# Kernel optimization log

Hardware: AMD Instinct MI355X
Metric: run time of the kernel (lower is better)

## Reference

```python
import jax, jax.numpy as jnp
import numpy as np

B, T, D = 4096, 8, 2048
EPS = 1e-5


def setup_inputs() -> dict:
    key = jax.random.key(0)
    ks = jax.random.split(key, 7)
    s = 1.0 / np.sqrt(D)  # xavier-ish scale
    return {
        "H": jax.random.normal(ks[0], (B, T, D), jnp.float32),
        "Wq": jax.random.normal(ks[1], (T, D, D), jnp.float32) * s,
        "Wk": jax.random.normal(ks[2], (D, D), jnp.float32) * s,
        "Wv": jax.random.normal(ks[3], (D, D), jnp.float32) * s,
        "Wg": jax.random.normal(ks[4], (T, D, D), jnp.float32) * s,
        "bg": jnp.zeros((T, D), jnp.float32),
        "gamma": jnp.ones((T, D), jnp.float32),
        "beta": jnp.zeros((T, D), jnp.float32),
    }


def reference(H, Wq, Wk, Wv, Wg, bg, gamma, beta):
    # H: (B, T, D) = stacked task_reprs. Linear uses y = x @ W.T.
    scale = jnp.sqrt(jnp.asarray(D, H.dtype))
    K = jnp.einsum('bsd,ed->bse', H, Wk)          # (B, T, D) shared keys
    V = jnp.einsum('bsd,ed->bse', H, Wv)          # (B, T, D) shared values
    Q = jnp.einsum('btd,ted->bte', H, Wq)         # per-task query projection
    scores = jnp.einsum('bte,bse->bts', Q, K) / scale  # (B, T, T)
    attn = jax.nn.softmax(scores, axis=-1)
    ctx = jnp.einsum('bts,bse->bte', attn, V)     # (B, T, D)
    # dropout is identity at eval time
    g = jax.nn.sigmoid(jnp.einsum('btd,ted->bte', H, Wg) + bg)  # per-task gate
    x = H + g * ctx                               # gated residual
    mu = jnp.mean(x, axis=-1, keepdims=True)
    var = jnp.var(x, axis=-1, keepdims=True)
    out = (x - mu) / jnp.sqrt(var + EPS) * gamma + beta  # per-task LayerNorm
    return out
```

## Files before the change

### kernel.cpp

```cpp
#include <hip/hip_runtime.h>
#include <cstdint>

typedef unsigned short u16;
typedef uint32_t u32;
typedef float f32x4 __attribute__((ext_vector_type(4)));
typedef __bf16 bf16x8 __attribute__((ext_vector_type(8)));

#define GLDS16(gp, lp)                                                                   \
  __builtin_amdgcn_global_load_lds((const __attribute__((address_space(1))) void*)(gp),  \
                                   (__attribute__((address_space(3))) void*)(lp), 16, 0, 0)

__device__ __forceinline__ float blo(u32 u) { return __uint_as_float(u << 16); }
__device__ __forceinline__ float bhi(u32 u) { return __uint_as_float(u & 0xFFFF0000u); }
__device__ __forceinline__ u16 f2b(float f) {
  u32 u = __float_as_uint(f);
  u32 r = u + 0x7FFFu + ((u >> 16) & 1u);
  return (u16)(r >> 16);
}

__global__ __launch_bounds__(256) void ctil_cvt_f2b(
    const float* __restrict__ in, u16* __restrict__ out, long n)
{
  long i = ((long)blockIdx.x * blockDim.x + threadIdx.x) * 8;
  const long stride = (long)gridDim.x * blockDim.x * 8;
  for (; i < n; i += stride) {
    float4 a = *reinterpret_cast<const float4*>(in + i);
    float4 b = *reinterpret_cast<const float4*>(in + i + 4);
    uint4 o;
    o.x = (u32)f2b(a.x) | ((u32)f2b(a.y) << 16);
    o.y = (u32)f2b(a.z) | ((u32)f2b(a.w) << 16);
    o.z = (u32)f2b(b.x) | ((u32)f2b(b.y) << 16);
    o.w = (u32)f2b(b.z) | ((u32)f2b(b.w) << 16);
    *reinterpret_cast<uint4*>(out + i) = o;
  }
}

__global__ __launch_bounds__(512, 2) void ctil_gemm256(
    const u16* __restrict__ Hb, const u16* __restrict__ Wqb,
    const u16* __restrict__ Wkb, const u16* __restrict__ Wvb,
    const u16* __restrict__ Wgb,
    u16* __restrict__ Kb, u16* __restrict__ Vb,
    u16* __restrict__ Qb, u16* __restrict__ Gb,
    int zbase)
{
  const int z = blockIdx.z + zbase;
  const u16* A;
  const u16* W;
  u16* C;
  int lda, ldc;
  if (z < 2) {
    A = Hb; lda = 2048; ldc = 2048;
    W = (z == 0) ? Wkb : Wvb;
    C = (z == 0) ? Kb : Vb;
  } else {
    const int t = (z - 2) & 7;
    A = Hb + t * 2048; lda = 16384; ldc = 16384;
    W = ((z < 10) ? Wqb : Wgb) + (size_t)t * (size_t)(2048 * 2048);
    C = ((z < 10) ? Qb : Gb) + t * 2048;
  }
  const int bm = blockIdx.x, bn = blockIdx.y;

  const int tid = (int)threadIdx.x;
  const int lane = tid & 63, wid = tid >> 6;
  const int wm = wid >> 2, wn = wid & 3;

  __shared__ __align__(16) u16 As[2][16384];
  __shared__ __align__(16) u16 Bs[2][16384];

  const int srl = lane >> 3;
  const int sq  = (lane & 7) ^ srl;
  const u16* Ag = A + (size_t)(bm * 256 + wid * 8 + srl) * lda + sq * 8;
  const u16* Bg = W + (size_t)(bn * 256 + wid * 8 + srl) * 2048 + sq * 8;

#define STAGE(buf, kt, h)                                                     \
  do {                                                                        \
    GLDS16(Ag + (size_t)((h) * 64) * lda + (kt) * 64,                         \
           &As[buf][((h) * 64 + wid * 8) * 64]);                              \
    GLDS16(Bg + (size_t)((h) * 64) * 2048 + (kt) * 64,                        \
           &Bs[buf][((h) * 64 + wid * 8) * 64]);                              \
  } while (0)

  const int la = lane & 15, g = lane >> 4, x = lane & 7;
  const int arow = wm * 128 + la;
  const int brow = wn * 64 + la;
  const int sl0 = (g ^ x) << 3;
  const int sl1 = ((4 | g) ^ x) << 3;

  bf16x8 aR[4][2];
  bf16x8 bR[2][2][2];
  f32x4 acc[8][4] = {};

#define DSA(buf, mh)                                                          \
  do {                                                                        \
    _Pragma("unroll") for (int j = 0; j < 4; ++j) {                           \
      const int r_ = (arow + (mh) * 64 + j * 16) * 64;                        \
      aR[j][0] = *reinterpret_cast<const bf16x8*>(&As[buf][r_ + sl0]);        \
      aR[j][1] = *reinterpret_cast<const bf16x8*>(&As[buf][r_ + sl1]);        \
    }                                                                         \
  } while (0)

#define DSB(buf, nh)                                                          \
  do {                                                                        \
    _Pragma("unroll") for (int j = 0; j < 2; ++j) {                           \
      const int r_ = (brow + (nh) * 32 + j * 16) * 64;                        \
      bR[nh][j][0] = *reinterpret_cast<const bf16x8*>(&Bs[buf][r_ + sl0]);    \
      bR[nh][j][1] = *reinterpret_cast<const bf16x8*>(&Bs[buf][r_ + sl1]);    \
    }                                                                         \
  } while (0)

#define MFMA16(mh, nh)                                                        \
  do {                                                                        \
    _Pragma("unroll") for (int j = 0; j < 4; ++j)                             \
    _Pragma("unroll") for (int jj = 0; jj < 2; ++jj)                          \
    _Pragma("unroll") for (int ks = 0; ks < 2; ++ks)                          \
      acc[(mh) * 4 + j][(nh) * 2 + jj] =                                      \
          __builtin_amdgcn_mfma_f32_16x16x32_bf16(                            \
              aR[j][ks], bR[nh][jj][ks], acc[(mh) * 4 + j][(nh) * 2 + jj],    \
              0, 0, 0);                                                       \
  } while (0)

#define BAR()                                                                 \
  do {                                                                        \
    __builtin_amdgcn_s_barrier();                                             \
    asm volatile("" ::: "memory");                                            \
  } while (0)
#define LGKMW() asm volatile("s_waitcnt lgkmcnt(0)" ::: "memory")
#define VMW(n) asm volatile("s_waitcnt vmcnt(" #n ")" ::: "memory")
#define PRIO_ON()  __builtin_amdgcn_s_setprio(1)
#define PRIO_OFF() __builtin_amdgcn_s_setprio(0)

#pragma unroll
  for (int h = 0; h < 4; ++h) STAGE(0, 0, h);
  STAGE(1, 1, 0);
  STAGE(1, 1, 1);
  VMW(4);
  BAR();

#pragma unroll 1
  for (int it = 0; it < 16; ++it) {
    const int k1 = 2 * it + 1, k2 = 2 * it + 2, k3 = 2 * it + 3;
    const bool nl = (it < 15);
    DSA(0, 0); DSB(0, 0);
    STAGE(1, k1, 2);
    STAGE(1, k1, 3);
    PRIO_ON(); MFMA16(0, 0); PRIO_OFF();
    BAR();
    DSB(0, 1);
    PRIO_ON(); MFMA16(0, 1); PRIO_OFF();
    BAR();
    DSA(0, 1);
    PRIO_ON(); MFMA16(1, 1); PRIO_OFF();
    LGKMW();
    BAR();
    if (nl) { STAGE(0, k2, 0); STAGE(0, k2, 1); }
    PRIO_ON(); MFMA16(1, 0); PRIO_OFF();
    if (nl) VMW(4); else VMW(0);
    BAR();
    DSA(1, 0); DSB(1, 0);
    if (nl) { STAGE(0, k2, 2); STAGE(0, k2, 3); }
    PRIO_ON(); MFMA16(0, 0); PRIO_OFF();
    BAR();
    DSB(1, 1);
    PRIO_ON(); MFMA16(0, 1); PRIO_OFF();
    BAR();
    DSA(1, 1);
    PRIO_ON(); MFMA16(1, 1); PRIO_OFF();
    LGKMW();
    BAR();
    if (nl) { STAGE(1, k3, 0); STAGE(1, k3, 1); }
    PRIO_ON(); MFMA16(1, 0); PRIO_OFF();
    if (nl) VMW(4); else VMW(0);
    BAR();
  }

  const int cl = lane & 15, cq = lane >> 4;
#pragma unroll
  for (int mf = 0; mf < 8; ++mf) {
#pragma unroll
    for (int r = 0; r < 4; ++r) {
      const int row = bm * 256 + wm * 128 + mf * 16 + cq * 4 + r;
      u16* Cr = C + (size_t)row * ldc + bn * 256 + wn * 64 + cl;
#pragma unroll
      for (int nf = 0; nf < 4; ++nf)
        Cr[nf * 16] = f2b(acc[mf][nf][r]);
    }
  }
#undef STAGE
#undef DSA
#undef DSB
#undef MFMA16
#undef BAR
#undef LGKMW
#undef VMW
}

__global__ __launch_bounds__(256) void ctil_epilogue(
    const u16* __restrict__ Hb, const u16* __restrict__ Kb,
    const u16* __restrict__ Vb, const u16* __restrict__ Qb,
    const u16* __restrict__ Gb, const float* __restrict__ bgp,
    const float* __restrict__ gap, const float* __restrict__ bep,
    float* __restrict__ Out)
{
  const int b = blockIdx.x;
  const int tid = (int)threadIdx.x;
  const int lane = tid & 63, wid = tid >> 6;
  const size_t rbase = (size_t)b * 16384;
  const int e0 = tid * 8;

  __shared__ float red[256];
  __shared__ float r1s[4], r2s[4];

  u32 qw[8][4], kw[8][4];
#pragma unroll
  for (int t = 0; t < 8; ++t) {
    uint4 v = *reinterpret_cast<const uint4*>(Qb + rbase + t * 2048 + e0);
    qw[t][0] = v.x; qw[t][1] = v.y; qw[t][2] = v.z; qw[t][3] = v.w;
    uint4 w = *reinterpret_cast<const uint4*>(Kb + rbase + t * 2048 + e0);
    kw[t][0] = w.x; kw[t][1] = w.y; kw[t][2] = w.z; kw[t][3] = w.w;
  }

  float sc[64];
#pragma unroll
  for (int p = 0; p < 64; ++p) sc[p] = 0.f;

#pragma unroll
  for (int c = 0; c < 4; ++c) {
    float ql[8], qh[8], kl[8], kh[8];
#pragma unroll
    for (int t = 0; t < 8; ++t) {
      ql[t] = blo(qw[t][c]); qh[t] = bhi(qw[t][c]);
      kl[t] = blo(kw[t][c]); kh[t] = bhi(kw[t][c]);
    }
#pragma unroll
    for (int t = 0; t < 8; ++t)
#pragma unroll
      for (int s = 0; s < 8; ++s)
        sc[t * 8 + s] += ql[t] * kl[s] + qh[t] * kh[s];
  }

#pragma unroll
  for (int p = 0; p < 64; ++p) {
    float v = sc[p];
#pragma unroll
    for (int m = 1; m < 64; m <<= 1) v += __shfl_xor(v, m, 64);
    sc[p] = v;
  }
  if (lane == 0) {
#pragma unroll
    for (int p = 0; p < 64; ++p) red[wid * 64 + p] = sc[p];
  }
  __syncthreads();

  const float INVS = 0.022097086912079608f;
#pragma unroll
  for (int p = 0; p < 64; ++p)
    sc[p] = (red[p] + red[64 + p] + red[128 + p] + red[192 + p]) * INVS;

#pragma unroll
  for (int t = 0; t < 8; ++t) {
    float m = sc[t * 8];
#pragma unroll
    for (int s = 1; s < 8; ++s) m = fmaxf(m, sc[t * 8 + s]);
    float l = 0.f;
#pragma unroll
    for (int s = 0; s < 8; ++s) {
      float e = __expf(sc[t * 8 + s] - m);
      sc[t * 8 + s] = e;
      l += e;
    }
    float inv = 1.f / l;
#pragma unroll
    for (int s = 0; s < 8; ++s) sc[t * 8 + s] *= inv;
  }

  u32 vw[8][4];
#pragma unroll
  for (int s = 0; s < 8; ++s) {
    uint4 v = *reinterpret_cast<const uint4*>(Vb + rbase + s * 2048 + e0);
    vw[s][0] = v.x; vw[s][1] = v.y; vw[s][2] = v.z; vw[s][3] = v.w;
  }

  for (int t = 0; t < 8; ++t) {
    float cx[8];
#pragma unroll
    for (int j = 0; j < 8; ++j) cx[j] = 0.f;
#pragma unroll
    for (int s = 0; s < 8; ++s) {
      float a = sc[t * 8 + s];
#pragma unroll
      for (int c = 0; c < 4; ++c) {
        cx[2 * c]     += a * blo(vw[s][c]);
        cx[2 * c + 1] += a * bhi(vw[s][c]);
      }
    }
    uint4 gu = *reinterpret_cast<const uint4*>(Gb + rbase + t * 2048 + e0);
    uint4 hu = *reinterpret_cast<const uint4*>(Hb + rbase + t * 2048 + e0);
    u32 ga[4] = {gu.x, gu.y, gu.z, gu.w};
    u32 ha[4] = {hu.x, hu.y, hu.z, hu.w};
    float bgv[8];
    *reinterpret_cast<float4*>(&bgv[0]) = *reinterpret_cast<const float4*>(bgp + t * 2048 + e0);
    *reinterpret_cast<float4*>(&bgv[4]) = *reinterpret_cast<const float4*>(bgp + t * 2048 + e0 + 4);
    float x[8];
    float s1 = 0.f, s2 = 0.f;
#pragma unroll
    for (int c = 0; c < 4; ++c) {
      float gl = blo(ga[c]) + bgv[2 * c];
      float gh = bhi(ga[c]) + bgv[2 * c + 1];
      float sgl = 1.f / (1.f + __expf(-gl));
      float sgh = 1.f / (1.f + __expf(-gh));
      float xl = blo(ha[c]) + sgl * cx[2 * c];
      float xh = bhi(ha[c]) + sgh * cx[2 * c + 1];
      x[2 * c] = xl; x[2 * c + 1] = xh;
      s1 += xl + xh;
      s2 += xl * xl + xh * xh;
    }
#pragma unroll
    for (int m = 1; m < 64; m <<= 1) {
      s1 += __shfl_xor(s1, m, 64);
      s2 += __shfl_xor(s2, m, 64);
    }
    if (lane == 0) { r1s[wid] = s1; r2s[wid] = s2; }
    __syncthreads();
    const float invD = 1.f / 2048.f;
    float S1 = r1s[0] + r1s[1] + r1s[2] + r1s[3];
    float S2 = r2s[0] + r2s[1] + r2s[2] + r2s[3];
    float mu = S1 * invD;
    float var = S2 * invD - mu * mu;
    float rstd = rsqrtf(var + 1e-5f);
    float gmv[8], btv[8];
    *reinterpret_cast<float4*>(&gmv[0]) = *reinterpret_cast<const float4*>(gap + t * 2048 + e0);
    *reinterpret_cast<float4*>(&gmv[4]) = *reinterpret_cast<const float4*>(gap + t * 2048 + e0 + 4);
    *reinterpret_cast<float4*>(&btv[0]) = *reinterpret_cast<const float4*>(bep + t * 2048 + e0);
    *reinterpret_cast<float4*>(&btv[4]) = *reinterpret_cast<const float4*>(bep + t * 2048 + e0 + 4);
    float4 o1, o2;
    o1.x = (x[0] - mu) * rstd * gmv[0] + btv[0];
    o1.y = (x[1] - mu) * rstd * gmv[1] + btv[1];
    o1.z = (x[2] - mu) * rstd * gmv[2] + btv[2];
    o1.w = (x[3] - mu) * rstd * gmv[3] + btv[3];
    o2.x = (x[4] - mu) * rstd * gmv[4] + btv[4];
    o2.y = (x[5] - mu) * rstd * gmv[5] + btv[5];
    o2.z = (x[6] - mu) * rstd * gmv[6] + btv[6];
    o2.w = (x[7] - mu) * rstd * gmv[7] + btv[7];
    *reinterpret_cast<float4*>(Out + rbase + t * 2048 + e0) = o1;
    *reinterpret_cast<float4*>(Out + rbase + t * 2048 + e0 + 4) = o2;
    __syncthreads();
  }
}

extern "C" void kernel_launch(void* const* d_in, const int* in_sizes, int n_in,
                              void* d_out, int out_size, void* d_ws, size_t ws_size,
                              hipStream_t stream)
{
  const float* H  = (const float*)d_in[0];
  const float* Wq = (const float*)d_in[1];
  const float* Wk = (const float*)d_in[2];
  const float* Wv = (const float*)d_in[3];
  const float* Wg = (const float*)d_in[4];
  const float* bg = (const float*)d_in[5];
  const float* ga = (const float*)d_in[6];
  const float* be = (const float*)d_in[7];
  float* Out = (float*)d_out;

  const size_t NWQ = 33554432, NWK = 4194304;
  u16* Wqb = (u16*)d_ws;
  u16* Wgb = Wqb + NWQ;
  u16* Wkb = Wgb + NWQ;
  u16* Wvb = Wkb + NWK;
  u16* chunkbase = Wvb + NWK;

  const size_t fixed = 150994944ull;
  int nch = 1;
  while (nch < 16 && fixed + (size_t)(4096 / nch) * 163840ull > ws_size) nch <<= 1;
  const int CB = 4096 / nch;

  u16* Hb = chunkbase;
  u16* Kw = Hb + (size_t)CB * 16384;
  u16* Vw = Kw + (size_t)CB * 16384;
  u16* Gw = Vw + (size_t)CB * 16384;
  u16* Qw = Gw + (size_t)CB * 16384;

  ctil_cvt_f2b<<<2048, 256, 0, stream>>>(Wq, Wqb, (long)NWQ);
  ctil_cvt_f2b<<<2048, 256, 0, stream>>>(Wg, Wgb, (long)NWQ);
  ctil_cvt_f2b<<<512, 256, 0, stream>>>(Wk, Wkb, (long)NWK);
  ctil_cvt_f2b<<<512, 256, 0, stream>>>(Wv, Wvb, (long)NWK);

  for (int c = 0; c < nch; ++c) {
    const size_t off = (size_t)c * (size_t)CB * 16384;
    ctil_cvt_f2b<<<2048, 256, 0, stream>>>(H + off, Hb, (long)CB * 16384);
    ctil_gemm256<<<dim3(CB / 32, 8, 2), 512, 0, stream>>>(
        Hb, Wqb, Wkb, Wvb, Wgb, Kw, Vw, Qw, Gw, 0);
    ctil_gemm256<<<dim3(CB / 256, 8, 16), 512, 0, stream>>>(
        Hb, Wqb, Wkb, Wvb, Wgb, Kw, Vw, Qw, Gw, 2);
    ctil_epilogue<<<dim3(CB), 256, 0, stream>>>(
        Hb, Kw, Vw, Qw, Gw, bg, ga, be, Out + off);
  }
}
```

Baseline: 1.583 ms.

## Double-buffer GEMM fragment registers and cut barriers in main loop

Splits the LDS fragment registers into two ping-pong sets so LDS reads for the next MFMA sub-tile overlap the current MFMAs. This reduces barriers per iteration from eight to two, and the prologue now stages both K tiles fully. The cost is higher VGPR pressure, which could lower occupancy or cause spills. Staging into a buffer while other waves may still be reading it risks races unless the barrier placement is exactly right.

```diff
diff --git a/kernel.cpp b/kernel.cpp
--- a/kernel.cpp
+++ b/kernel.cpp
@@ -86,36 +86,36 @@
   const int sl0 = (g ^ x) << 3;
   const int sl1 = ((4 | g) ^ x) << 3;
 
-  bf16x8 aR[4][2];
-  bf16x8 bR[2][2][2];
+  bf16x8 a0[4][2], a1[4][2];
+  bf16x8 b0[2][2], b1[2][2];
   f32x4 acc[8][4] = {};
 
-#define DSA(buf, mh)                                                          \
+#define DSA(buf, mh, dst)                                                     \
   do {                                                                        \
     _Pragma("unroll") for (int j = 0; j < 4; ++j) {                           \
       const int r_ = (arow + (mh) * 64 + j * 16) * 64;                        \
-      aR[j][0] = *reinterpret_cast<const bf16x8*>(&As[buf][r_ + sl0]);        \
-      aR[j][1] = *reinterpret_cast<const bf16x8*>(&As[buf][r_ + sl1]);        \
+      dst[j][0] = *reinterpret_cast<const bf16x8*>(&As[buf][r_ + sl0]);       \
+      dst[j][1] = *reinterpret_cast<const bf16x8*>(&As[buf][r_ + sl1]);       \
     }                                                                         \
   } while (0)
 
-#define DSB(buf, nh)                                                          \
+#define DSB(buf, nh, dst)                                                     \
   do {                                                                        \
     _Pragma("unroll") for (int j = 0; j < 2; ++j) {                           \
       const int r_ = (brow + (nh) * 32 + j * 16) * 64;                        \
-      bR[nh][j][0] = *reinterpret_cast<const bf16x8*>(&Bs[buf][r_ + sl0]);    \
-      bR[nh][j][1] = *reinterpret_cast<const bf16x8*>(&Bs[buf][r_ + sl1]);    \
+      dst[j][0] = *reinterpret_cast<const bf16x8*>(&Bs[buf][r_ + sl0]);       \
+      dst[j][1] = *reinterpret_cast<const bf16x8*>(&Bs[buf][r_ + sl1]);       \
     }                                                                         \
   } while (0)
 
-#define MFMA16(mh, nh)                                                        \
+#define MFMA16(Aa, Bb, mh, nh)                                                \
   do {                                                                        \
     _Pragma("unroll") for (int j = 0; j < 4; ++j)                             \
     _Pragma("unroll") for (int jj = 0; jj < 2; ++jj)                          \
     _Pragma("unroll") for (int ks = 0; ks < 2; ++ks)                          \
       acc[(mh) * 4 + j][(nh) * 2 + jj] =                                      \
           __builtin_amdgcn_mfma_f32_16x16x32_bf16(                            \
-              aR[j][ks], bR[nh][jj][ks], acc[(mh) * 4 + j][(nh) * 2 + jj],    \
+              Aa[j][ks], Bb[jj][ks], acc[(mh) * 4 + j][(nh) * 2 + jj],        \
               0, 0, 0);                                                       \
   } while (0)
 
@@ -131,46 +131,39 @@
 
 #pragma unroll
   for (int h = 0; h < 4; ++h) STAGE(0, 0, h);
-  STAGE(1, 1, 0);
-  STAGE(1, 1, 1);
-  VMW(4);
+#pragma unroll
+  for (int h = 0; h < 4; ++h) STAGE(1, 1, h);
+  VMW(8);
   BAR();
+  DSA(0, 0, a0);
+  DSB(0, 0, b0);
 
 #pragma unroll 1
   for (int it = 0; it < 16; ++it) {
-    const int k1 = 2 * it + 1, k2 = 2 * it + 2, k3 = 2 * it + 3;
+    const int k2 = 2 * it + 2, k3 = 2 * it + 3;
     const bool nl = (it < 15);
-    DSA(0, 0); DSB(0, 0);
-    STAGE(1, k1, 2);
-    STAGE(1, k1, 3);
-    PRIO_ON(); MFMA16(0, 0); PRIO_OFF();
-    BAR();
-    DSB(0, 1);
-    PRIO_ON(); MFMA16(0, 1); PRIO_OFF();
-    BAR();
-    DSA(0, 1);
-    PRIO_ON(); MFMA16(1, 1); PRIO_OFF();
-    LGKMW();
-    BAR();
+    DSA(0, 1, a1);
+    PRIO_ON(); MFMA16(a0, b0, 0, 0); PRIO_OFF();
+    DSB(0, 1, b1);
+    PRIO_ON(); MFMA16(a1, b0, 1, 0); PRIO_OFF();
+    LGKMW(); VMW(0); BAR();
     if (nl) { STAGE(0, k2, 0); STAGE(0, k2, 1); }
-    PRIO_ON(); MFMA16(1, 0); PRIO_OFF();
-    if (nl) VMW(4); else VMW(0);
-    BAR();
-    DSA(1, 0); DSB(1, 0);
+    DSB(1, 0, b0);
+    PRIO_ON(); MFMA16(a0, b1, 0, 1); PRIO_OFF();
     if (nl) { STAGE(0, k2, 2); STAGE(0, k2, 3); }
-    PRIO_ON(); MFMA16(0, 0); PRIO_OFF();
-    BAR();
-    DSB(1, 1);
-    PRIO_ON(); MFMA16(0, 1); PRIO_OFF();
-    BAR();
-    DSA(1, 1);
-    PRIO_ON(); MFMA16(1, 1); PRIO_OFF();
-    LGKMW();
-    BAR();
+    DSA(1, 0, a0);
+    PRIO_ON(); MFMA16(a1, b1, 1, 1); PRIO_OFF();
+    DSA(1, 1, a1);
+    PRIO_ON(); MFMA16(a0, b0, 0, 0); PRIO_OFF();
+    DSB(1, 1, b1);
+    PRIO_ON(); MFMA16(a1, b0, 1, 0); PRIO_OFF();
+    LGKMW(); VMW(0); BAR();
     if (nl) { STAGE(1, k3, 0); STAGE(1, k3, 1); }
-    PRIO_ON(); MFMA16(1, 0); PRIO_OFF();
-    if (nl) VMW(4); else VMW(0);
-    BAR();
+    if (nl) DSB(0, 0, b0);
+    PRIO_ON(); MFMA16(a0, b1, 0, 1); PRIO_OFF();
+    if (nl) { STAGE(1, k3, 2); STAGE(1, k3, 3); }
+    if (nl) DSA(0, 0, a0);
+    PRIO_ON(); MFMA16(a1, b1, 1, 1); PRIO_OFF();
   }
 
   const int cl = lane & 15, cq = lane >> 4;
```

After: 1.603 ms. Within noise of the previous version (+1.2%).
